# Kernel tuning notes

Hardware: AMD Instinct MI355X
Metric: run time of the kernel (lower is better)

## Reference

```python
import jax, jax.numpy as jnp
import numpy as np

NUM_HEADS = 16
HEAD_DIM = 64  # 1024 / 16


def setup_inputs() -> dict:
    key = jax.random.key(0)
    ks = jax.random.split(key, 8)
    B, S, D = 2, 2048, 1024
    s = 0.02
    return {
        "hidden_states_q": jax.random.normal(ks[0], (B, S, D), jnp.float32),
        "hidden_states_k": jax.random.normal(ks[1], (B, S, D), jnp.float32),
        "hidden_states_v": jax.random.normal(ks[2], (B, S, D), jnp.float32),
        "Wq": jax.random.normal(ks[3], (D, D), jnp.float32) * s,
        "bq": jnp.zeros((D,), jnp.float32),
        "Wk": jax.random.normal(ks[4], (D, D), jnp.float32) * s,
        "bk": jnp.zeros((D,), jnp.float32),
        "Wv": jax.random.normal(ks[5], (D, D), jnp.float32) * s,
        "bv": jnp.zeros((D,), jnp.float32),
        "Wp": jax.random.normal(ks[6], (D, D), jnp.float32) * s,
        "bp": jnp.zeros((D,), jnp.float32),
    }


def _split_heads(x):
    B, S, D = x.shape
    return x.reshape(B, S, NUM_HEADS, HEAD_DIM).transpose(0, 2, 1, 3)  # [B,H,S,dh]


def reference(hidden_states_q, hidden_states_k, hidden_states_v,
              Wq, bq, Wk, bk, Wv, bv, Wp, bp):
    # Projections (Linear / Conv1D are both x @ W + b in this parameterization)
    q = _split_heads(hidden_states_q @ Wq + bq)
    k = _split_heads(hidden_states_k @ Wk + bk)
    v = _split_heads(hidden_states_v @ Wv + bv)
    scale = 1.0 / jnp.sqrt(jnp.asarray(HEAD_DIM, q.dtype))
    # NOTE: no causal mask is applied in the original _attn (mask asserted None)
    attn = jnp.einsum("bhqd,bhkd->bhqk", q, k) * scale
    attn = jax.nn.softmax(attn, axis=-1)  # attn_dropout is identity in eval
    out = jnp.einsum("bhqk,bhkd->bhqd", attn, v)
    B, H, S, dh = out.shape
    out = out.transpose(0, 2, 1, 3).reshape(B, S, H * dh)
    out = out @ Wp + bp  # resid_dropout identity in eval
    return out
```

## Files before the change

kernel.cpp:

```cpp
#include <hip/hip_runtime.h>
#include <stdint.h>


typedef _Float16 f16;
typedef __attribute__((ext_vector_type(8))) _Float16 f16x8;
typedef __attribute__((ext_vector_type(4))) _Float16 f16x4;
typedef __attribute__((ext_vector_type(4))) float f32x4;
typedef __attribute__((ext_vector_type(16))) float f32x16;
typedef __attribute__((ext_vector_type(2))) unsigned u32x2;

#define NB 2
#define SEQ 2048
#define DMODEL 1024
#define NH 16
#define DH 64

#define QSCALE 0.1803368801111601f

__device__ __forceinline__ void gload_lds16(const void* g, void* l) {
  __builtin_amdgcn_global_load_lds(
      (const __attribute__((address_space(1))) unsigned int*)g,
      (__attribute__((address_space(3))) unsigned int*)l, 16, 0, 0);
}

__device__ __forceinline__ void plswap(unsigned& a, unsigned& b) {
  u32x2 r = __builtin_amdgcn_permlane32_swap(a, b, false, false);
  a = r[0];
  b = r[1];
}

__global__ __launch_bounds__(256) void cast_f16_3(
    const float* __restrict__ s0, const float* __restrict__ s1,
    const float* __restrict__ s2, f16* __restrict__ d0, f16* __restrict__ d1,
    f16* __restrict__ d2) {
  const float* src = blockIdx.z == 0 ? s0 : (blockIdx.z == 1 ? s1 : s2);
  f16* dst = blockIdx.z == 0 ? d0 : (blockIdx.z == 1 ? d1 : d2);
  int i = (blockIdx.x * 256 + threadIdx.x) * 8;
  float4 a = *(const float4*)(src + i);
  float4 b = *(const float4*)(src + i + 4);
  f16x8 o;
  o[0] = (f16)a.x; o[1] = (f16)a.y; o[2] = (f16)a.z; o[3] = (f16)a.w;
  o[4] = (f16)b.x; o[5] = (f16)b.y; o[6] = (f16)b.z; o[7] = (f16)b.w;
  *(f16x8*)(dst + i) = o;
}

__global__ __launch_bounds__(256) void transw(
    const float* __restrict__ w0, const float* __restrict__ w1,
    const float* __restrict__ w2, const float* __restrict__ w3,
    f16* __restrict__ t0, f16* __restrict__ t1, f16* __restrict__ t2,
    f16* __restrict__ t3) {
  __shared__ float tile[64][65];
  const float* W; f16* T;
  switch (blockIdx.z) {
    case 0: W = w0; T = t0; break;
    case 1: W = w1; T = t1; break;
    case 2: W = w2; T = t2; break;
    default: W = w3; T = t3; break;
  }
  int r0 = blockIdx.y * 64, c0 = blockIdx.x * 64;
  for (int it = 0; it < 16; ++it) {
    int idx = it * 256 + threadIdx.x;
    int r = idx >> 6, c = idx & 63;
    tile[r][c] = W[(size_t)(r0 + r) * DMODEL + c0 + c];
  }
  __syncthreads();
  for (int it = 0; it < 16; ++it) {
    int idx = it * 256 + threadIdx.x;
    int r = idx >> 6, c = idx & 63;
    T[(size_t)(c0 + r) * DMODEL + r0 + c] = (f16)tile[c][r];
  }
}

__global__ __launch_bounds__(256) void gemm128(
    const f16* __restrict__ xq, const f16* __restrict__ xk,
    const f16* __restrict__ xv, const f16* __restrict__ ao,
    const f16* __restrict__ wqt, const f16* __restrict__ wkt,
    const f16* __restrict__ wvt, const f16* __restrict__ wpt,
    const float* __restrict__ bq, const float* __restrict__ bk,
    const float* __restrict__ bv, const float* __restrict__ bp,
    f16* __restrict__ qo, f16* __restrict__ ko, f16* __restrict__ vto,
    float* __restrict__ out, int mode_base) {
  __shared__ char lds[32768];
  char* ldsA = lds;
  char* ldsB = lds + 16384;

  int mode = mode_base + blockIdx.z;
  const f16* Am; const f16* Bt; const float* bias; float oscale = 1.0f;
  if (mode == 0)      { Am = xq; Bt = wqt; bias = bq; oscale = QSCALE; }
  else if (mode == 1) { Am = xk; Bt = wkt; bias = bk; }
  else if (mode == 2) { Am = xv; Bt = wvt; bias = bv; }
  else                { Am = ao; Bt = wpt; bias = bp; }

  const int tid = threadIdx.x;
  const int l = tid & 63, w = tid >> 6;
  const int g = l >> 4, c = l & 15;
  const int wr = w >> 1, wc = w & 1;
  const int m0 = blockIdx.y * 128, n0 = blockIdx.x * 128;

  const int srow = w * 8 + (l >> 3);
  const int schunk = (l & 7) ^ ((l >> 3) & 7);

  f32x4 acc[4][4] = {};

  for (int k0 = 0; k0 < DMODEL; k0 += 64) {
#pragma unroll
    for (int it = 0; it < 4; ++it) {
      int row = it * 32 + srow;
      gload_lds16(Am + (size_t)(m0 + row) * DMODEL + k0 + schunk * 8,
                  ldsA + it * 4096 + w * 1024);
    }
#pragma unroll
    for (int it = 0; it < 4; ++it) {
      int row = it * 32 + srow;
      gload_lds16(Bt + (size_t)(n0 + row) * DMODEL + k0 + schunk * 8,
                  ldsB + it * 4096 + w * 1024);
    }
    __syncthreads();
    f16x8 af[2][4], bf[2][4];
#pragma unroll
    for (int kc = 0; kc < 2; ++kc)
#pragma unroll
      for (int i = 0; i < 4; ++i) {
        int row = wr * 64 + i * 16 + c;
        af[kc][i] = *(const f16x8*)(ldsA + row * 128 + (((kc * 4 + g) ^ (row & 7)) << 4));
        int rowb = wc * 64 + i * 16 + c;
        bf[kc][i] = *(const f16x8*)(ldsB + rowb * 128 + (((kc * 4 + g) ^ (rowb & 7)) << 4));
      }
#pragma unroll
    for (int kc = 0; kc < 2; ++kc)
#pragma unroll
      for (int i = 0; i < 4; ++i)
#pragma unroll
        for (int j = 0; j < 4; ++j)
          acc[i][j] = __builtin_amdgcn_mfma_f32_16x16x32_f16(af[kc][i], bf[kc][j],
                                                             acc[i][j], 0, 0, 0);
    __syncthreads();
  }

#pragma unroll
  for (int i = 0; i < 4; ++i) {
#pragma unroll
    for (int j = 0; j < 4; ++j) {
      int grb = m0 + wr * 64 + i * 16 + g * 4;
      int gc = n0 + wc * 64 + j * 16 + c;
      float bval = bias[gc];
      if (mode == 3) {
#pragma unroll
        for (int e = 0; e < 4; ++e)
          out[(size_t)(grb + e) * DMODEL + gc] = acc[i][j][e] + bval;
      } else if (mode == 2) {
        int b = grb >> 11, s = grb & 2047, h = gc >> 6, d = gc & 63;
        f16x4 pk;
#pragma unroll
        for (int e = 0; e < 4; ++e) pk[e] = (f16)(acc[i][j][e] + bval);
        *(f16x4*)(vto + ((size_t)((b * NH + h) * DH + d)) * SEQ + s) = pk;
      } else {
        f16* dst = (mode == 0) ? qo : ko;
        int b = grb >> 11, s = grb & 2047, h = gc >> 6, d = gc & 63;
#pragma unroll
        for (int e = 0; e < 4; ++e)
          dst[(((size_t)(b * NH + h) * SEQ) + (s + e)) * DH + d] =
              (f16)((acc[i][j][e] + bval) * oscale);
      }
    }
  }
}

__global__ __launch_bounds__(256, 4) void attn64(
    const f16* __restrict__ qg, const f16* __restrict__ kg,
    const f16* __restrict__ vtg, f16* __restrict__ aout) {
  __shared__ char lds[32768];

  const int tid = threadIdx.x;
  const int l = tid & 63, w = tid >> 6;
  const int q31 = l & 31;
  const bool hi = l >= 32;
  const int p = w & 1;
  const int qgrp = w >> 1;

  const int bid = blockIdx.x;
  const int bh = (bid & 7) + 8 * (bid >> 8);
  const int qc = (bid >> 3) & 31;
  const int q0 = qc * 64 + qgrp * 32;

  f16x8 qf[4];
#pragma unroll
  for (int ks = 0; ks < 4; ++ks)
    qf[ks] = *(const f16x8*)(qg + ((size_t)bh * SEQ + q0 + q31) * DH + ks * 16 +
                             (hi ? 8 : 0));

  float lsum = 0.0f;
  f32x16 oacc[2] = {};

  const int srow = w * 8 + (l >> 3);
  const int schunk = (l & 7) ^ ((l >> 3) & 7);

  auto stage = [&](int buf, int t) {
    char* baseK = lds + buf * 16384;
    char* baseV = baseK + 8192;
#pragma unroll
    for (int it = 0; it < 2; ++it) {
      int row = it * 32 + srow;
      gload_lds16(kg + ((size_t)bh * SEQ + t * 64 + row) * DH + schunk * 8,
                  baseK + it * 4096 + w * 1024);
      gload_lds16(vtg + ((size_t)bh * DH + row) * SEQ + t * 64 + schunk * 8,
                  baseV + it * 4096 + w * 1024);
    }
  };

  stage(0, 0);
  __syncthreads();

  for (int t = 0; t < 32; ++t) {
    int cur = t & 1;
    if (t + 1 < 32) stage(cur ^ 1, t + 1);

    const char* ldsK = lds + cur * 16384;
    const char* ldsV = ldsK + 8192;

    f32x16 st = {};
    __builtin_amdgcn_s_setprio(1);
#pragma unroll
    for (int ks = 0; ks < 4; ++ks) {
      int row = p * 32 + q31;
      int ch = ((ks * 2 + (hi ? 1 : 0)) ^ (q31 & 7)) << 4;
      f16x8 kf = *(const f16x8*)(ldsK + row * 128 + ch);
      st = __builtin_amdgcn_mfma_f32_32x32x16_f16(kf, qf[ks], st, 0, 0, 0);
    }
    __builtin_amdgcn_s_setprio(0);

    float ps[16];
#pragma unroll
    for (int r = 0; r < 16; ++r) ps[r] = exp2f(st[r]);
#pragma unroll
    for (int r = 0; r < 16; ++r) lsum += ps[r];
    unsigned dw[8];
#pragma unroll
    for (int i = 0; i < 8; ++i)
      dw[i] = __builtin_bit_cast(
          unsigned, __builtin_amdgcn_cvt_pkrtz(ps[2 * i], ps[2 * i + 1]));
    plswap(dw[0], dw[2]);
    plswap(dw[1], dw[3]);
    plswap(dw[4], dw[6]);
    plswap(dw[5], dw[7]);

    __builtin_amdgcn_s_setprio(1);
#pragma unroll
    for (int ks2 = 0; ks2 < 2; ++ks2) {
      union { unsigned u[4]; f16x8 v; } pb;
      pb.u[0] = dw[ks2 * 4 + 0];
      pb.u[1] = dw[ks2 * 4 + 1];
      pb.u[2] = dw[ks2 * 4 + 2];
      pb.u[3] = dw[ks2 * 4 + 3];
#pragma unroll
      for (int dt = 0; dt < 2; ++dt) {
        int vrow = dt * 32 + q31;
        int ch = ((p * 4 + ks2 * 2 + (hi ? 1 : 0)) ^ (vrow & 7)) << 4;
        f16x8 vf = *(const f16x8*)(ldsV + vrow * 128 + ch);
        oacc[dt] = __builtin_amdgcn_mfma_f32_32x32x16_f16(vf, pb.v, oacc[dt], 0, 0, 0);
      }
    }
    __builtin_amdgcn_s_setprio(0);
    __syncthreads();
  }

  __syncthreads();
  char* reg = lds + qgrp * 9216;
  if (p == 1) {
#pragma unroll
    for (int j = 0; j < 8; ++j) {
      f32x4 ck;
#pragma unroll
      for (int e = 0; e < 4; ++e) ck[e] = oacc[j >> 2][(j & 3) * 4 + e];
      *(f32x4*)(reg + j * 1024 + l * 16) = ck;
    }
    *(float*)(reg + 8192 + l * 4) = lsum;
  }
  __syncthreads();
  if (p == 0) {
#pragma unroll
    for (int j = 0; j < 8; ++j) {
      f32x4 ck = *(const f32x4*)(reg + j * 1024 + l * 16);
#pragma unroll
      for (int e = 0; e < 4; ++e) oacc[j >> 2][(j & 3) * 4 + e] += ck[e];
    }
    float lt = lsum + *(const float*)(reg + 8192 + l * 4);
    lt += __shfl_xor(lt, 32);
    float inv = 1.0f / lt;
    const int b = bh >> 4, h = bh & 15;
    const int s = q0 + q31;
#pragma unroll
    for (int dt = 0; dt < 2; ++dt)
#pragma unroll
      for (int rg = 0; rg < 4; ++rg) {
        f16x4 pk;
#pragma unroll
        for (int j = 0; j < 4; ++j) pk[j] = (f16)(oacc[dt][rg * 4 + j] * inv);
        int d0 = dt * 32 + rg * 8 + (hi ? 4 : 0);
        *(f16x4*)(aout + ((size_t)(b * SEQ + s)) * DMODEL + h * DH + d0) = pk;
      }
  }
}

extern "C" void kernel_launch(void* const* d_in, const int* in_sizes, int n_in,
                              void* d_out, int out_size, void* d_ws, size_t ws_size,
                              hipStream_t stream) {
  const float* hq = (const float*)d_in[0];
  const float* hk = (const float*)d_in[1];
  const float* hv = (const float*)d_in[2];
  const float* Wq = (const float*)d_in[3];
  const float* bq = (const float*)d_in[4];
  const float* Wk = (const float*)d_in[5];
  const float* bk = (const float*)d_in[6];
  const float* Wv = (const float*)d_in[7];
  const float* bv = (const float*)d_in[8];
  const float* Wp = (const float*)d_in[9];
  const float* bp = (const float*)d_in[10];
  float* out = (float*)d_out;

  f16* xq  = (f16*)d_ws;
  f16* xk  = xq + 4194304;
  f16* xv  = xk + 4194304;
  f16* wqt = xv + 4194304;
  f16* wkt = wqt + 1048576;
  f16* wvt = wkt + 1048576;
  f16* wpt = wvt + 1048576;
  f16* qb  = wpt + 1048576;
  f16* kb  = qb + 4194304;
  f16* vtb = kb + 4194304;
  f16* ao  = vtb + 4194304;

  cast_f16_3<<<dim3(2048, 1, 3), 256, 0, stream>>>(hq, hk, hv, xq, xk, xv);
  transw<<<dim3(16, 16, 4), 256, 0, stream>>>(Wq, Wk, Wv, Wp, wqt, wkt, wvt, wpt);
  gemm128<<<dim3(8, 32, 3), 256, 0, stream>>>(xq, xk, xv, ao, wqt, wkt, wvt, wpt,
                                              bq, bk, bv, bp, qb, kb, vtb, out, 0);
  attn64<<<dim3(1024), 256, 0, stream>>>(qb, kb, vtb, ao);
  gemm128<<<dim3(8, 32, 1), 256, 0, stream>>>(xq, xk, xv, ao, wqt, wkt, wvt, wpt,
                                              bq, bk, bv, bp, qb, kb, vtb, out, 3);
}
```

Baseline: 156.1 us.

## Load K/V fragments directly from global memory, dropping LDS double buffering

Removes the LDS staging of K and V tiles, their double-buffered async loads and the per-iteration block barriers. Each wave now reads its MFMA fragments for K and transposed V straight from global memory into registers, relying on L2/cache reuse across waves that share the same K/V tile. The LDS allocation shrinks to what the final cross-wave reduction needs, which could raise occupancy. In exchange there is more global/L2 traffic because two q-groups read the same data, and each iteration exposes load latency without explicit prefetch beyond what unroll-by-2 lets the compiler schedule.

```diff
diff --git a/kernel.cpp b/kernel.cpp
--- a/kernel.cpp
+++ b/kernel.cpp
@@ -169,7 +169,7 @@
 __global__ __launch_bounds__(256, 4) void attn64(
     const f16* __restrict__ qg, const f16* __restrict__ kg,
     const f16* __restrict__ vtg, f16* __restrict__ aout) {
-  __shared__ char lds[32768];
+  __shared__ char lds[2 * 9216];
 
   const int tid = threadIdx.x;
   const int l = tid & 63, w = tid >> 6;
@@ -192,41 +192,28 @@
   float lsum = 0.0f;
   f32x16 oacc[2] = {};
 
-  const int srow = w * 8 + (l >> 3);
-  const int schunk = (l & 7) ^ ((l >> 3) & 7);
-
-  auto stage = [&](int buf, int t) {
-    char* baseK = lds + buf * 16384;
-    char* baseV = baseK + 8192;
-#pragma unroll
-    for (int it = 0; it < 2; ++it) {
-      int row = it * 32 + srow;
-      gload_lds16(kg + ((size_t)bh * SEQ + t * 64 + row) * DH + schunk * 8,
-                  baseK + it * 4096 + w * 1024);
-      gload_lds16(vtg + ((size_t)bh * DH + row) * SEQ + t * 64 + schunk * 8,
-                  baseV + it * 4096 + w * 1024);
-    }
-  };
-
-  stage(0, 0);
-  __syncthreads();
-
+  const f16* kb = kg + ((size_t)bh * SEQ + p * 32 + q31) * DH + (hi ? 8 : 0);
+  const f16* vb = vtg + ((size_t)bh * DH + q31) * SEQ + p * 32 + (hi ? 8 : 0);
+
+#pragma unroll 2
   for (int t = 0; t < 32; ++t) {
-    int cur = t & 1;
-    if (t + 1 < 32) stage(cur ^ 1, t + 1);
-
-    const char* ldsK = lds + cur * 16384;
-    const char* ldsV = ldsK + 8192;
+    const f16* kp = kb + (size_t)t * 64 * DH;
+    const f16* vp = vb + t * 64;
+    f16x8 vf00 = *(const f16x8*)(vp);
+    f16x8 vf01 = *(const f16x8*)(vp + 16);
+    f16x8 vf10 = *(const f16x8*)(vp + (size_t)32 * SEQ);
+    f16x8 vf11 = *(const f16x8*)(vp + (size_t)32 * SEQ + 16);
+    f16x8 kf0 = *(const f16x8*)(kp);
+    f16x8 kf1 = *(const f16x8*)(kp + 16);
+    f16x8 kf2 = *(const f16x8*)(kp + 32);
+    f16x8 kf3 = *(const f16x8*)(kp + 48);
 
     f32x16 st = {};
     __builtin_amdgcn_s_setprio(1);
-#pragma unroll
-    for (int ks = 0; ks < 4; ++ks) {
-      int row = p * 32 + q31;
-      int ch = ((ks * 2 + (hi ? 1 : 0)) ^ (q31 & 7)) << 4;
-      f16x8 kf = *(const f16x8*)(ldsK + row * 128 + ch);
-      st = __builtin_amdgcn_mfma_f32_32x32x16_f16(kf, qf[ks], st, 0, 0, 0);
-    }
+    st = __builtin_amdgcn_mfma_f32_32x32x16_f16(kf0, qf[0], st, 0, 0, 0);
+    st = __builtin_amdgcn_mfma_f32_32x32x16_f16(kf1, qf[1], st, 0, 0, 0);
+    st = __builtin_amdgcn_mfma_f32_32x32x16_f16(kf2, qf[2], st, 0, 0, 0);
+    st = __builtin_amdgcn_mfma_f32_32x32x16_f16(kf3, qf[3], st, 0, 0, 0);
     __builtin_amdgcn_s_setprio(0);
 
     float ps[16];
@@ -244,27 +231,18 @@
     plswap(dw[4], dw[6]);
     plswap(dw[5], dw[7]);
 
+    union { unsigned u[4]; f16x8 v; } pb0, pb1;
+    pb0.u[0] = dw[0]; pb0.u[1] = dw[1]; pb0.u[2] = dw[2]; pb0.u[3] = dw[3];
+    pb1.u[0] = dw[4]; pb1.u[1] = dw[5]; pb1.u[2] = dw[6]; pb1.u[3] = dw[7];
+
     __builtin_amdgcn_s_setprio(1);
-#pragma unroll
-    for (int ks2 = 0; ks2 < 2; ++ks2) {
-      union { unsigned u[4]; f16x8 v; } pb;
-      pb.u[0] = dw[ks2 * 4 + 0];
-      pb.u[1] = dw[ks2 * 4 + 1];
-      pb.u[2] = dw[ks2 * 4 + 2];
-      pb.u[3] = dw[ks2 * 4 + 3];
-#pragma unroll
-      for (int dt = 0; dt < 2; ++dt) {
-        int vrow = dt * 32 + q31;
-        int ch = ((p * 4 + ks2 * 2 + (hi ? 1 : 0)) ^ (vrow & 7)) << 4;
-        f16x8 vf = *(const f16x8*)(ldsV + vrow * 128 + ch);
-        oacc[dt] = __builtin_amdgcn_mfma_f32_32x32x16_f16(vf, pb.v, oacc[dt], 0, 0, 0);
-      }
-    }
+    oacc[0] = __builtin_amdgcn_mfma_f32_32x32x16_f16(vf00, pb0.v, oacc[0], 0, 0, 0);
+    oacc[1] = __builtin_amdgcn_mfma_f32_32x32x16_f16(vf10, pb0.v, oacc[1], 0, 0, 0);
+    oacc[0] = __builtin_amdgcn_mfma_f32_32x32x16_f16(vf01, pb1.v, oacc[0], 0, 0, 0);
+    oacc[1] = __builtin_amdgcn_mfma_f32_32x32x16_f16(vf11, pb1.v, oacc[1], 0, 0, 0);
     __builtin_amdgcn_s_setprio(0);
-    __syncthreads();
-  }
-
-  __syncthreads();
+  }
+
   char* reg = lds + qgrp * 9216;
   if (p == 1) {
 #pragma unroll
```

New measurement: 215.2 us. +37.9%, slower.
